# Kernel optimization log

Hardware: AMD Instinct MI355X
Metric: run time of the kernel (lower is better)

The kernel has to match this reference:

```python
import jax, jax.numpy as jnp
import numpy as np

N = 1_000_000   # nodes / batch_size
E = 8_000_000   # positive edges
EPS = 1e-8


def normalize_points(p):
    """Normalize projective points: unit-norm features, sign-fixed homogeneous coord."""
    feats = p[..., :-1]
    hom = p[..., -1:]
    zero = jnp.all(feats == 0, axis=-1, keepdims=True)
    feats = jnp.where(zero, jnp.ones_like(feats), feats)
    nrm = jnp.sqrt(jnp.sum(feats * feats, axis=-1, keepdims=True))
    nf = feats / jnp.maximum(nrm, EPS)
    out = jnp.concatenate([nf, hom], axis=-1)
    sgn = jnp.sign(out[..., -1:])
    sgn = jnp.where(sgn == 0, jnp.ones_like(sgn), sgn)
    return out * sgn


def get_ideal_points(line):
    """Ideal points: intersect line l=(a,b,c) (l.p=0) with the null cone x^2+y^2=z^2 (z=1 chart)."""
    a, b, c = line[..., 0], line[..., 1], line[..., 2]
    n2 = jnp.maximum(a * a + b * b, EPS)
    x0, y0 = -c * a / n2, -c * b / n2              # closest point of chord to origin
    t = jnp.sqrt(jnp.maximum(1.0 - c * c / n2, 0.0))  # half chord length (clamped)
    inv = 1.0 / jnp.sqrt(n2)
    px, py = -b * inv, a * inv                     # unit direction along the chord
    one = jnp.ones_like(a)
    i1 = jnp.stack([x0 + t * px, y0 + t * py, one], axis=-1)
    i2 = jnp.stack([x0 - t * px, y0 - t * py, one], axis=-1)
    return i1, i2


def cross_ratio(p1, p2, p3, p4):
    p1, p2, p3, p4 = (normalize_points(p) for p in (p1, p2, p3, p4))
    d = lambda a, b: jnp.sqrt(jnp.sum((a - b) ** 2, axis=-1))
    cr = (d(p1, p2) * d(p3, p4)) / (d(p1, p3) * d(p2, p4) + EPS)
    return jnp.clip(cr, -5.0, 5.0)


def edge_points(z_proj, src, dst):
    p1, p2 = z_proj[src], z_proj[dst]
    line = jnp.cross(p1, p2)  # join of two projective points in 3D
    i1, i2 = get_ideal_points(line)
    return p1, p2, i1, i2


def setup_inputs():
    key = jax.random.key(0)
    k1, k2, k3, k4 = jax.random.split(key, 4)
    return {
        "z": jax.random.normal(k1, (N, 2), dtype=jnp.float32),
        "edge_index": jax.random.randint(k2, (2, E), 0, N, dtype=jnp.int32),
        "neg_edge_index": jax.random.randint(k3, (2, N), 0, N, dtype=jnp.int32),
        "reg_indices": jax.random.randint(k4, (10,), 0, N, dtype=jnp.int32),
        "batch_size": N,
    }


def reference(z, edge_index, neg_edge_index, reg_indices, batch_size):
    z_proj = jnp.concatenate([z, jnp.ones_like(z[..., :1])], axis=-1)  # [N,3]
    z_proj = normalize_points(z_proj)

    # positive edges (masked mean, matching torch filtering + division by count)
    mask = ((edge_index[0] < batch_size) & (edge_index[1] < batch_size)).astype(z.dtype)
    p1, p2, i1, i2 = edge_points(z_proj, edge_index[0], edge_index[1])
    cr_pos = cross_ratio(p1, p2, i1, i2)
    pos_loss = jnp.sum(jax.nn.softplus(-cr_pos) * mask) / jnp.maximum(jnp.sum(mask), 1.0)

    # negative edges (target 0)
    p1, p2, i1, i2 = edge_points(z_proj, neg_edge_index[0], neg_edge_index[1])
    neg_loss = jnp.mean(jax.nn.softplus(cross_ratio(p1, p2, i1, i2)))

    # cross-ratio involution regularizer over all pairs of sampled nodes
    ns = reg_indices.shape[0]
    ii, jj = np.triu_indices(ns, k=1)
    p1, p2, i1, i2 = edge_points(z_proj, reg_indices[ii], reg_indices[jj])
    cr1 = cross_ratio(p1, p2, i1, i2)
    cr2 = cross_ratio(i1, i2, p1, p2)
    reg_loss = jnp.sum(jnp.abs(cr1 * cr2 - 1.0)) / (ns * (ns - 1) / 2)

    total = pos_loss + neg_loss + 0.1 * reg_loss
    return jnp.clip(total, 0.0, 5.0)
```

## Files before the change

### kernel.cpp

```cpp
#include <hip/hip_runtime.h>

#define EPSF 1e-8f
#define EPT 16

typedef int iv4 __attribute__((ext_vector_type(4)));

__device__ __forceinline__ float frcp(float x) { return __builtin_amdgcn_rcpf(x); }
__device__ __forceinline__ float frsq(float x) { return __builtin_amdgcn_rsqf(x); }
__device__ __forceinline__ float sq(float x) { return x * x; }

__device__ __forceinline__ float sp_neg(float x) {
    return 0.69314718f * __builtin_amdgcn_logf(1.0f + __builtin_amdgcn_exp2f(-x * 1.44269504f));
}

__device__ __forceinline__ float2 norm_pt(float x, float y) {
    if (x == 0.0f && y == 0.0f) { x = 1.0f; y = 1.0f; }
    float nrm = sqrtf(x * x + y * y);
    float inv = frcp(fmaxf(nrm, EPSF));
    return make_float2(x * inv, y * inv);
}

__device__ __forceinline__ float edge_cr_full(float x1, float y1, float x2, float y2) {
    float a = y1 - y2;
    float b = x2 - x1;
    float c = x1 * y2 - y1 * x2;
    float n2 = fmaxf(a * a + b * b, EPSF);
    float rn2 = frcp(n2);
    float x0 = -c * a * rn2;
    float y0 = -c * b * rn2;
    float t  = sqrtf(fmaxf(1.0f - c * c * rn2, 0.0f));
    float inv = frsq(n2);
    float px = -b * inv, py = a * inv;
    float2 q1 = norm_pt(x0 + t * px, y0 + t * py);
    float2 q2 = norm_pt(x0 - t * px, y0 - t * py);
    float d12 = sqrtf(sq(x1 - x2)   + sq(y1 - y2));
    float d34 = sqrtf(sq(q1.x - q2.x) + sq(q1.y - q2.y));
    float d13 = sqrtf(sq(x1 - q1.x) + sq(y1 - q1.y));
    float d24 = sqrtf(sq(x2 - q2.x) + sq(y2 - q2.y));
    float cr = d12 * d34 * frcp(d13 * d24 + EPSF);
    return fminf(fmaxf(cr, -5.0f), 5.0f);
}

__device__ __forceinline__ void block_reduce2(float v0, float v1, double* a0, double* a1) {
    #pragma unroll
    for (int o = 32; o > 0; o >>= 1) {
        v0 += __shfl_down(v0, o, 64);
        v1 += __shfl_down(v1, o, 64);
    }
    __shared__ float s0[8], s1[8];
    int lane = threadIdx.x & 63, wid = threadIdx.x >> 6;
    if (lane == 0) { s0[wid] = v0; s1[wid] = v1; }
    __syncthreads();
    if (threadIdx.x == 0) {
        float t0 = 0.0f, t1 = 0.0f;
        int nw = blockDim.x >> 6;
        for (int w = 0; w < nw; ++w) { t0 += s0[w]; t1 += s1[w]; }
        atomicAdd(a0, (double)t0);
        if (a1) atomicAdd(a1, (double)t1);
    }
}

__global__ void norm_kernel(const float* __restrict__ z, unsigned short* __restrict__ tab, int N) {
    int stride = gridDim.x * blockDim.x;
    for (int i = blockIdx.x * blockDim.x + threadIdx.x; i < N; i += stride) {
        float2 p = ((const float2*)z)[i];
        float x = p.x, y = p.y;
        if (x == 0.0f && y == 0.0f) { x = 1.0f; y = 1.0f; }
        float ang = atan2f(y, x);
        int u = (int)lrintf(ang * 10430.378350470453f);
        tab[i] = (unsigned short)(u & 0xFFFF);
    }
}

template <bool USE_TAB>
__global__ __launch_bounds__(256)
void edge_kernel(const unsigned short* __restrict__ tab, const float* __restrict__ z,
                 const int* __restrict__ ei, int E,
                 const int* __restrict__ nei, int En,
                 const int* __restrict__ bsp, int N, int gp,
                 double* __restrict__ acc) {
    const bool is_pos = (int)blockIdx.x < gp;
    const int* idx;
    int cnt, blk0;
    if (is_pos) { idx = ei;  cnt = E;  blk0 = blockIdx.x; }
    else        { idx = nei; cnt = En; blk0 = blockIdx.x - gp; }
    const int* src = idx;
    const int* dst = idx + cnt;
    const int bs = bsp[0];
    const unsigned nm1 = (unsigned)(N - 1);

    float lsum = 0.0f, lcnt = 0.0f;
    long long base = ((long long)blk0 * blockDim.x + threadIdx.x) * EPT;

    if (base + EPT <= (long long)cnt) {
        iv4 s4[EPT / 4], d4[EPT / 4];
        #pragma unroll
        for (int k = 0; k < EPT / 4; ++k) {
            s4[k] = __builtin_nontemporal_load((const iv4*)(src + base) + k);
            d4[k] = __builtin_nontemporal_load((const iv4*)(dst + base) + k);
        }
        unsigned short ua[EPT], ub[EPT];
        float2 fa[EPT], fb[EPT];
        #pragma unroll
        for (int k = 0; k < EPT; ++k) {
            unsigned si = min((unsigned)s4[k >> 2][k & 3], nm1);
            unsigned di = min((unsigned)d4[k >> 2][k & 3], nm1);
            if (USE_TAB) {
                ua[k] = tab[si];
                ub[k] = tab[di];
            } else {
                fa[k] = ((const float2*)z)[si];
                fb[k] = ((const float2*)z)[di];
            }
        }
        #pragma unroll
        for (int k = 0; k < EPT; ++k) {
            float d2;
            if (USE_TAB) {
                int du = (short)(unsigned short)(ua[k] - ub[k]);
                float s = __sinf((float)du * 4.7936899621426287e-5f);
                d2 = 4.0f * s * s;
            } else {
                float2 pa = norm_pt(fa[k].x, fa[k].y);
                float2 pb = norm_pt(fb[k].x, fb[k].y);
                float dx = pa.x - pb.x, dy = pa.y - pb.y;
                d2 = dx * dx + dy * dy;
            }
            float cr = fminf(d2 * 1e8f, 5.0f);
            float t = sp_neg(cr);
            if (is_pos) {
                int s = s4[k >> 2][k & 3], d = d4[k >> 2][k & 3];
                float m = (s < bs && d < bs) ? 1.0f : 0.0f;
                lsum += t * m;
                lcnt += m;
            } else {
                lsum += cr + t;
            }
        }
    } else {
        for (long long i = base; i < (long long)cnt; ++i) {
            int s = src[i], d = dst[i];
            unsigned si = min((unsigned)s, nm1);
            unsigned di = min((unsigned)d, nm1);
            float d2;
            if (USE_TAB) {
                int du = (short)(unsigned short)(tab[si] - tab[di]);
                float ss = __sinf((float)du * 4.7936899621426287e-5f);
                d2 = 4.0f * ss * ss;
            } else {
                float2 a = ((const float2*)z)[si];
                float2 b = ((const float2*)z)[di];
                float2 pa = norm_pt(a.x, a.y);
                float2 pb = norm_pt(b.x, b.y);
                float dx = pa.x - pb.x, dy = pa.y - pb.y;
                d2 = dx * dx + dy * dy;
            }
            float cr = fminf(d2 * 1e8f, 5.0f);
            float t = sp_neg(cr);
            if (is_pos) {
                float m = (s < bs && d < bs) ? 1.0f : 0.0f;
                lsum += t * m; lcnt += m;
            } else {
                lsum += cr + t;
            }
        }
    }

    if (is_pos) block_reduce2(lsum, lcnt, &acc[0], &acc[1]);
    else        block_reduce2(lsum, 0.0f, &acc[2], nullptr);
}

__global__ void reg_fin_kernel(const float* __restrict__ z, const int* __restrict__ ridx,
                               int nreg, int N, const double* __restrict__ acc,
                               float* __restrict__ out, int nneg) {
    int t = threadIdx.x;
    int npairs = nreg * (nreg - 1) / 2;
    float v = 0.0f;
    for (int p = t; p < npairs; p += 64) {
        int idx = p, i = 0, cnt = nreg - 1;
        while (idx >= cnt) { idx -= cnt; ++i; --cnt; }
        int j = i + 1 + idx;
        unsigned si = min((unsigned)ridx[i], (unsigned)(N - 1));
        unsigned di = min((unsigned)ridx[j], (unsigned)(N - 1));
        float2 zs = *(const float2*)(z + 2u * si);
        float2 zd = *(const float2*)(z + 2u * di);
        float2 p1 = norm_pt(zs.x, zs.y);
        float2 p2 = norm_pt(zd.x, zd.y);
        float cr = edge_cr_full(p1.x, p1.y, p2.x, p2.y);
        v += fabsf(cr * cr - 1.0f);
    }
    #pragma unroll
    for (int o = 32; o > 0; o >>= 1) v += __shfl_down(v, o, 64);
    if (t == 0) {
        double pos = acc[0] / fmax(acc[1], 1.0);
        double neg = acc[2] / (double)nneg;
        double reg = (double)v / (double)npairs;
        double tot = pos + neg + 0.1 * reg;
        tot = fmin(fmax(tot, 0.0), 5.0);
        out[0] = (float)tot;
    }
}

extern "C" void kernel_launch(void* const* d_in, const int* in_sizes, int n_in,
                              void* d_out, int out_size, void* d_ws, size_t ws_size,
                              hipStream_t stream) {
    const float* z  = (const float*)d_in[0];
    const int* ei   = (const int*)d_in[1];
    const int* nei  = (const int*)d_in[2];
    const int* ridx = (const int*)d_in[3];
    const int* bsp  = (const int*)d_in[4];
    float* out = (float*)d_out;

    int N    = in_sizes[0] / 2;
    int E    = in_sizes[1] / 2;
    int Nn   = in_sizes[2] / 2;
    int nreg = in_sizes[3];

    double* acc = (double*)d_ws;
    unsigned short* tab = (unsigned short*)((char*)d_ws + 256);
    size_t need = 256 + (size_t)N * sizeof(unsigned short);
    bool use_tab = (ws_size >= need);

    (void)hipMemsetAsync(acc, 0, 4 * sizeof(double), stream);

    const int threads = 256;
    const long long per_blk = (long long)threads * EPT;
    int gp = (int)((E  + per_blk - 1) / per_blk);
    int gn = (int)((Nn + per_blk - 1) / per_blk);

    if (use_tab) {
        int gnorm = (N + threads * 4 - 1) / (threads * 4); if (gnorm > 1024) gnorm = 1024;
        norm_kernel<<<gnorm, threads, 0, stream>>>(z, tab, N);
        edge_kernel<true><<<gp + gn, threads, 0, stream>>>(tab, z, ei, E, nei, Nn, bsp, N, gp, acc);
    } else {
        edge_kernel<false><<<gp + gn, threads, 0, stream>>>(nullptr, z, ei, E, nei, Nn, bsp, N, gp, acc);
    }
    reg_fin_kernel<<<1, 64, 0, stream>>>(z, ridx, nreg, N, acc, out, Nn);
}
```

Before: 109.6 us.

## Fold accumulator reset into norm kernel and finalize in last edge block

Removes the hipMemsetAsync by zeroing the accumulators and a new completion counter inside norm_kernel. The separate reg/finalize kernel is dropped: each edge block bumps an atomic counter after its reduction, and the last block computes the regularizer and writes the final loss. This cuts two launches and their gaps, at the cost of an extra atomic and fence per block and a serialized tail in the final block.

```diff
diff --git a/kernel.cpp b/kernel.cpp
--- a/kernel.cpp
+++ b/kernel.cpp
@@ -60,7 +60,12 @@
     }
 }
 
-__global__ void norm_kernel(const float* __restrict__ z, unsigned short* __restrict__ tab, int N) {
+__global__ void norm_kernel(const float* __restrict__ z, unsigned short* __restrict__ tab,
+                            int N, double* __restrict__ acc, unsigned* __restrict__ counter) {
+    if (blockIdx.x == 0 && threadIdx.x == 0) {
+        acc[0] = 0.0; acc[1] = 0.0; acc[2] = 0.0; acc[3] = 0.0;
+        *counter = 0u;
+    }
     int stride = gridDim.x * blockDim.x;
     for (int i = blockIdx.x * blockDim.x + threadIdx.x; i < N; i += stride) {
         float2 p = ((const float2*)z)[i];
@@ -78,7 +83,9 @@
                  const int* __restrict__ ei, int E,
                  const int* __restrict__ nei, int En,
                  const int* __restrict__ bsp, int N, int gp,
-                 double* __restrict__ acc) {
+                 double* __restrict__ acc, unsigned* __restrict__ counter,
+                 const int* __restrict__ ridx, int nreg,
+                 float* __restrict__ out) {
     const bool is_pos = (int)blockIdx.x < gp;
     const int* idx;
     int cnt, blk0;
@@ -168,36 +175,44 @@
 
     if (is_pos) block_reduce2(lsum, lcnt, &acc[0], &acc[1]);
     else        block_reduce2(lsum, 0.0f, &acc[2], nullptr);
-}
-
-__global__ void reg_fin_kernel(const float* __restrict__ z, const int* __restrict__ ridx,
-                               int nreg, int N, const double* __restrict__ acc,
-                               float* __restrict__ out, int nneg) {
-    int t = threadIdx.x;
-    int npairs = nreg * (nreg - 1) / 2;
-    float v = 0.0f;
-    for (int p = t; p < npairs; p += 64) {
-        int idx = p, i = 0, cnt = nreg - 1;
-        while (idx >= cnt) { idx -= cnt; ++i; --cnt; }
-        int j = i + 1 + idx;
-        unsigned si = min((unsigned)ridx[i], (unsigned)(N - 1));
-        unsigned di = min((unsigned)ridx[j], (unsigned)(N - 1));
-        float2 zs = *(const float2*)(z + 2u * si);
-        float2 zd = *(const float2*)(z + 2u * di);
-        float2 p1 = norm_pt(zs.x, zs.y);
-        float2 p2 = norm_pt(zd.x, zd.y);
-        float cr = edge_cr_full(p1.x, p1.y, p2.x, p2.y);
-        v += fabsf(cr * cr - 1.0f);
-    }
-    #pragma unroll
-    for (int o = 32; o > 0; o >>= 1) v += __shfl_down(v, o, 64);
-    if (t == 0) {
-        double pos = acc[0] / fmax(acc[1], 1.0);
-        double neg = acc[2] / (double)nneg;
-        double reg = (double)v / (double)npairs;
-        double tot = pos + neg + 0.1 * reg;
-        tot = fmin(fmax(tot, 0.0), 5.0);
-        out[0] = (float)tot;
+
+    __shared__ int s_last;
+    if (threadIdx.x == 0) {
+        __threadfence();
+        unsigned prev = atomicAdd(counter, 1u);
+        s_last = (prev == (unsigned)(gridDim.x - 1)) ? 1 : 0;
+    }
+    __syncthreads();
+    if (s_last && threadIdx.x < 64) {
+        __threadfence();
+        int npairs = nreg * (nreg - 1) / 2;
+        float v = 0.0f;
+        for (int p = threadIdx.x; p < npairs; p += 64) {
+            int idx2 = p, i = 0, c2 = nreg - 1;
+            while (idx2 >= c2) { idx2 -= c2; ++i; --c2; }
+            int j = i + 1 + idx2;
+            unsigned si = min((unsigned)ridx[i], nm1);
+            unsigned di = min((unsigned)ridx[j], nm1);
+            float2 zs = ((const float2*)z)[si];
+            float2 zd = ((const float2*)z)[di];
+            float2 p1 = norm_pt(zs.x, zs.y);
+            float2 p2 = norm_pt(zd.x, zd.y);
+            float cr = edge_cr_full(p1.x, p1.y, p2.x, p2.y);
+            v += fabsf(cr * cr - 1.0f);
+        }
+        #pragma unroll
+        for (int o = 32; o > 0; o >>= 1) v += __shfl_down(v, o, 64);
+        if (threadIdx.x == 0) {
+            double pos_s = atomicAdd(&acc[0], 0.0);
+            double pos_c = atomicAdd(&acc[1], 0.0);
+            double neg_s = atomicAdd(&acc[2], 0.0);
+            double pos = pos_s / fmax(pos_c, 1.0);
+            double neg = neg_s / (double)En;
+            double reg = (double)v / (double)npairs;
+            double tot = pos + neg + 0.1 * reg;
+            tot = fmin(fmax(tot, 0.0), 5.0);
+            out[0] = (float)tot;
+        }
     }
 }
 
@@ -217,23 +232,25 @@
     int nreg = in_sizes[3];
 
     double* acc = (double*)d_ws;
+    unsigned* counter = (unsigned*)((char*)d_ws + 64);
     unsigned short* tab = (unsigned short*)((char*)d_ws + 256);
     size_t need = 256 + (size_t)N * sizeof(unsigned short);
     bool use_tab = (ws_size >= need);
-
-    (void)hipMemsetAsync(acc, 0, 4 * sizeof(double), stream);
 
     const int threads = 256;
     const long long per_blk = (long long)threads * EPT;
     int gp = (int)((E  + per_blk - 1) / per_blk);
     int gn = (int)((Nn + per_blk - 1) / per_blk);
 
+    int gnorm = (N + threads * 4 - 1) / (threads * 4); if (gnorm > 1024) gnorm = 1024;
+    if (gnorm < 1) gnorm = 1;
+    norm_kernel<<<gnorm, threads, 0, stream>>>(z, tab, use_tab ? N : 0, acc, counter);
+
     if (use_tab) {
-        int gnorm = (N + threads * 4 - 1) / (threads * 4); if (gnorm > 1024) gnorm = 1024;
-        norm_kernel<<<gnorm, threads, 0, stream>>>(z, tab, N);
-        edge_kernel<true><<<gp + gn, threads, 0, stream>>>(tab, z, ei, E, nei, Nn, bsp, N, gp, acc);
+        edge_kernel<true><<<gp + gn, threads, 0, stream>>>(tab, z, ei, E, nei, Nn, bsp, N, gp,
+                                                           acc, counter, ridx, nreg, out);
     } else {
-        edge_kernel<false><<<gp + gn, threads, 0, stream>>>(nullptr, z, ei, E, nei, Nn, bsp, N, gp, acc);
-    }
-    reg_fin_kernel<<<1, 64, 0, stream>>>(z, ridx, nreg, N, acc, out, Nn);
-}
+        edge_kernel<false><<<gp + gn, threads, 0, stream>>>(nullptr, z, ei, E, nei, Nn, bsp, N, gp,
+                                                            acc, counter, ridx, nreg, out);
+    }
+}
```

New measurement: 185.1 us. 69.0% more time.
